# Optimization experiments

Hardware: AMD Instinct MI355X
Metric: run time of the kernel (lower is better)

Reference implementation:

```python
import jax, jax.numpy as jnp
import numpy as np

V, E, H, S = 32000, 1024, 1024, 2048


def setup_inputs() -> dict:
    key = jax.random.key(0)
    ks = jax.random.split(key, 16)
    std = 0.02
    return {
        "encoder_out": jax.random.normal(ks[0], (S, E), jnp.float32),
        "word_input": jax.random.randint(ks[1], (1,), 0, V, jnp.int32),
        "last_context": jax.random.normal(ks[2], (1, H), jnp.float32),
        "h0": jnp.zeros((1, 1, H), jnp.float32),
        "c0": jnp.zeros((1, 1, H), jnp.float32),
        # learned parameters
        "emb": jax.random.normal(ks[3], (V, E), jnp.float32) * std,
        "W_ih": jax.random.normal(ks[4], (4 * H, E + H), jnp.float32) * std,
        "W_hh": jax.random.normal(ks[5], (4 * H, H), jnp.float32) * std,
        "b_ih": jnp.zeros((4 * H,), jnp.float32),
        "b_hh": jnp.zeros((4 * H,), jnp.float32),
        "W_attn": jax.random.normal(ks[6], (H, E + H), jnp.float32) * std,
        "b_attn": jnp.zeros((H,), jnp.float32),
        "v": jax.random.uniform(ks[7], (H,), jnp.float32) * 0.1,
        "W_ah": jax.random.normal(ks[8], (H, E + H), jnp.float32) * std,
        "b_ah": jnp.zeros((H,), jnp.float32),
        "W_out": jax.random.normal(ks[9], (V, H), jnp.float32) * std,
        "b_out": jnp.zeros((V,), jnp.float32),
    }


def reference(encoder_out, word_input, last_context, h0, c0,
              emb, W_ih, W_hh, b_ih, b_hh,
              W_attn, b_attn, v, W_ah, b_ah, W_out, b_out):
    # single decoder step, batch=1 (dropout in eval mode == identity)
    embedded = emb[word_input[0]]                       # [E]
    x = jnp.concatenate([last_context[0], embedded])    # [H+E] (context first, as in torch.cat)
    # LSTM cell (PyTorch gate order i, f, g, o)
    gates = W_ih @ x + b_ih + W_hh @ h0[0, 0] + b_hh    # [4H]
    i, f, g, o = jnp.split(gates, 4)
    c = jax.nn.sigmoid(f) * c0[0, 0] + jax.nn.sigmoid(i) * jnp.tanh(g)
    ht = jax.nn.sigmoid(o) * jnp.tanh(c)                # [H]
    # additive attention, vectorized over encoder steps.
    # original concatenates (ht, encoder_out[i]); split attn weight accordingly.
    Wa_h, Wa_e = W_attn[:, :H], W_attn[:, H:]
    scores = jnp.tanh(encoder_out @ Wa_e.T + (Wa_h @ ht + b_attn)) @ v  # [S]
    w = jax.nn.softmax(scores)                          # [S]
    context = w @ encoder_out                           # [E]
    ht_tilda = jnp.tanh(W_ah @ jnp.concatenate([context, ht]) + b_ah)  # [H]
    output = jax.nn.log_softmax(W_out @ ht_tilda + b_out)              # [V]
    return (output[None, :], (ht[None, None, :], c[None, None, :]),
            ht_tilda[None, :], w[None, :])
```

## Files before the change

### kernel.cpp

```cpp
#include <hip/hip_runtime.h>
#include <math.h>

#define V_ 32000
#define E_ 1024
#define H_ 1024
#define S_ 2048

typedef __attribute__((ext_vector_type(8))) short bf16x8;
typedef __attribute__((ext_vector_type(8))) unsigned short u16x8;
typedef __attribute__((ext_vector_type(4))) float f32x4;

typedef __attribute__((address_space(1))) const unsigned int gu32;
typedef __attribute__((address_space(3))) unsigned int lu32;

__device__ __forceinline__ float sigmoidf_(float x) { return 1.0f / (1.0f + expf(-x)); }

__device__ __forceinline__ unsigned short f2bf(float f) {
    unsigned int u = __builtin_bit_cast(unsigned int, f);
    unsigned int r = (u + 0x7fffu + ((u >> 16) & 1u)) >> 16;
    return (unsigned short)r;
}
__device__ __forceinline__ float bf2f(unsigned short u) {
    return __builtin_bit_cast(float, ((unsigned int)u) << 16);
}
__device__ __forceinline__ u16x8 pack8(float4 a, float4 b) {
    u16x8 p;
    p[0] = f2bf(a.x); p[1] = f2bf(a.y); p[2] = f2bf(a.z); p[3] = f2bf(a.w);
    p[4] = f2bf(b.x); p[5] = f2bf(b.y); p[6] = f2bf(b.z); p[7] = f2bf(b.w);
    return p;
}
__device__ __forceinline__ void gload16(const void* g, void* l) {
    __builtin_amdgcn_global_load_lds((gu32*)g, (lu32*)l, 16, 0, 0);
}

__global__ __launch_bounds__(256) void kA(
    const float* __restrict__ W_ih, const float* __restrict__ W_hh,
    const float* __restrict__ b_ih, const float* __restrict__ b_hh,
    const float* __restrict__ last_context, const float* __restrict__ emb,
    const int* __restrict__ word, const float* __restrict__ h0,
    const float* __restrict__ c0, const float* __restrict__ enc,
    const float* __restrict__ W_attn,
    float* __restrict__ out_ht, float* __restrict__ out_c,
    float* __restrict__ ws_ht, unsigned short* __restrict__ encb,
    unsigned short* __restrict__ wab, float* __restrict__ ws_ctx)
{
    int b = blockIdx.x, tid = threadIdx.x;
    int wave = tid >> 6, lane = tid & 63;
    if (b < 1024) {
        __shared__ float sbuf[4];
        int j = b;
        const float* embrow = emb + (size_t)word[0] * E_;
        int row = j + wave * H_;
        const float* wi = W_ih + (size_t)row * (E_ + H_);
        const float* wh = W_hh + (size_t)row * H_;
        float acc = 0.f;
        #pragma unroll
        for (int it = 0; it < 8; ++it) {
            int idx = (lane + it * 64) * 4;
            float4 wv = *(const float4*)(wi + idx);
            float4 xv = (idx < H_) ? *(const float4*)(last_context + idx)
                                   : *(const float4*)(embrow + (idx - H_));
            acc = fmaf(wv.x, xv.x, acc); acc = fmaf(wv.y, xv.y, acc);
            acc = fmaf(wv.z, xv.z, acc); acc = fmaf(wv.w, xv.w, acc);
        }
        #pragma unroll
        for (int it = 0; it < 4; ++it) {
            int idx = (lane + it * 64) * 4;
            float4 wv = *(const float4*)(wh + idx);
            float4 hv = *(const float4*)(h0 + idx);
            acc = fmaf(wv.x, hv.x, acc); acc = fmaf(wv.y, hv.y, acc);
            acc = fmaf(wv.z, hv.z, acc); acc = fmaf(wv.w, hv.w, acc);
        }
        #pragma unroll
        for (int m = 32; m; m >>= 1) acc += __shfl_down(acc, m, 64);
        if (lane == 0) sbuf[wave] = acc;
        __syncthreads();
        if (tid < 4 && b == 0) {
        }
        if (tid == 0) {
            float gi = sbuf[0] + b_ih[j]          + b_hh[j];
            float gf = sbuf[1] + b_ih[j + H_]     + b_hh[j + H_];
            float gg = sbuf[2] + b_ih[j + 2*H_]   + b_hh[j + 2*H_];
            float go = sbuf[3] + b_ih[j + 3*H_]   + b_hh[j + 3*H_];
            float c  = sigmoidf_(gf) * c0[j] + sigmoidf_(gi) * tanhf(gg);
            float ht = sigmoidf_(go) * tanhf(c);
            out_c[j]  = c;
            out_ht[j] = ht;
            ws_ht[j]  = ht;
        }
        if (b == 0) {
            ws_ctx[tid] = 0.f;
            ws_ctx[tid + 256] = 0.f;
            ws_ctx[tid + 512] = 0.f;
            ws_ctx[tid + 768] = 0.f;
        }
    } else {
        int cid = (b - 1024) * 256 + tid;
        const int ENC_CH = (S_ * E_) / 8;
        #pragma unroll
        for (int i = 0; i < 3; ++i) {
            int idx = cid + i * 131072;
            const float* src;
            unsigned short* dst;
            if (idx < ENC_CH) {
                src = enc + (size_t)idx * 8;
                dst = encb + (size_t)idx * 8;
            } else {
                int w = idx - ENC_CH;
                int h = w >> 7, off = (w & 127) * 8;
                src = W_attn + (size_t)h * (E_ + H_) + H_ + off;
                dst = wab + (size_t)h * E_ + off;
            }
            float4 a = *(const float4*)src;
            float4 bq = *(const float4*)(src + 4);
            *(u16x8*)dst = pack8(a, bq);
        }
    }
}

__global__ __launch_bounds__(64) void kB(
    const float* __restrict__ W_attn, const float* __restrict__ b_attn,
    const float* __restrict__ ht, float* __restrict__ q)
{
    int h = blockIdx.x;
    int lane = threadIdx.x;
    const float* row = W_attn + (size_t)h * (E_ + H_);
    float acc = 0.f;
    #pragma unroll
    for (int it = 0; it < 4; ++it) {
        int idx = (lane + it * 64) * 4;
        float4 wv = *(const float4*)(row + idx);
        float4 hv = *(const float4*)(ht + idx);
        acc = fmaf(wv.x, hv.x, acc); acc = fmaf(wv.y, hv.y, acc);
        acc = fmaf(wv.z, hv.z, acc); acc = fmaf(wv.w, hv.w, acc);
    }
    #pragma unroll
    for (int m = 32; m; m >>= 1) acc += __shfl_down(acc, m, 64);
    if (lane == 0) q[h] = acc + b_attn[h];
}

__global__ __launch_bounds__(256) void kC(
    const unsigned short* __restrict__ encb, const unsigned short* __restrict__ wab,
    const float* __restrict__ q, const float* __restrict__ v,
    float* __restrict__ spart)
{
    __shared__ unsigned short As[2][128 * 64];
    __shared__ unsigned short Bs[2][64 * 64];
    int s0 = blockIdx.x * 128, h0 = blockIdx.y * 64;
    int tid = threadIdx.x;
    int wave = tid >> 6, lane = tid & 63;
    int wr = (wave >> 1) * 64, wc = (wave & 1) * 32;

    int srow = tid >> 3;
    int lch  = ((tid & 7) ^ (srow & 7)) * 8;
    const unsigned short* aSrc[4];
    #pragma unroll
    for (int jj = 0; jj < 4; ++jj)
        aSrc[jj] = encb + (size_t)(s0 + jj * 32 + srow) * E_ + lch;
    const unsigned short* bSrc[2];
    #pragma unroll
    for (int jj = 0; jj < 2; ++jj)
        bSrc[jj] = wab + (size_t)(h0 + jj * 32 + srow) * E_ + lch;

    int fc = lane & 15, g = lane >> 4;
    int aRow[4], bRow[2], pc[2];
    #pragma unroll
    for (int m = 0; m < 4; ++m) aRow[m] = (wr + m * 16 + fc) * 64;
    #pragma unroll
    for (int n = 0; n < 2; ++n) bRow[n] = (wc + n * 16 + fc) * 64;
    #pragma unroll
    for (int kk = 0; kk < 2; ++kk) pc[kk] = ((kk * 4 + g) ^ (fc & 7)) * 8;

    f32x4 acc[4][2];
    #pragma unroll
    for (int m = 0; m < 4; ++m)
        #pragma unroll
        for (int n = 0; n < 2; ++n)
            acc[m][n] = (f32x4){0.f, 0.f, 0.f, 0.f};

    #pragma unroll
    for (int jj = 0; jj < 4; ++jj) gload16(aSrc[jj], &As[0][jj * 2048 + tid * 8]);
    #pragma unroll
    for (int jj = 0; jj < 2; ++jj) gload16(bSrc[jj], &Bs[0][jj * 2048 + tid * 8]);
    __syncthreads();

    int cur = 0;
    for (int t = 0; t < 16; ++t) {
        if (t < 15) {
            int k0 = (t + 1) * 64;
            #pragma unroll
            for (int jj = 0; jj < 4; ++jj)
                gload16(aSrc[jj] + k0, &As[cur ^ 1][jj * 2048 + tid * 8]);
            #pragma unroll
            for (int jj = 0; jj < 2; ++jj)
                gload16(bSrc[jj] + k0, &Bs[cur ^ 1][jj * 2048 + tid * 8]);
        }
        #pragma unroll
        for (int kk = 0; kk < 2; ++kk) {
            bf16x8 af[4], bf2[2];
            #pragma unroll
            for (int m = 0; m < 4; ++m) af[m] = *(const bf16x8*)&As[cur][aRow[m] + pc[kk]];
            #pragma unroll
            for (int n = 0; n < 2; ++n) bf2[n] = *(const bf16x8*)&Bs[cur][bRow[n] + pc[kk]];
            #pragma unroll
            for (int m = 0; m < 4; ++m)
                #pragma unroll
                for (int n = 0; n < 2; ++n)
                    acc[m][n] = __builtin_amdgcn_mfma_f32_16x16x32_bf16(
                        af[m], bf2[n], acc[m][n], 0, 0, 0);
        }
        __syncthreads();
        cur ^= 1;
    }

    float qv[2], vv[2];
    #pragma unroll
    for (int n = 0; n < 2; ++n) {
        int col = h0 + wc + n * 16 + fc;
        qv[n] = q[col];
        vv[n] = v[col];
    }
    int part = blockIdx.y * 2 + (wave & 1);
    #pragma unroll
    for (int m = 0; m < 4; ++m) {
        #pragma unroll
        for (int j = 0; j < 4; ++j) {
            float p = 0.f;
            #pragma unroll
            for (int n = 0; n < 2; ++n)
                p += tanhf(acc[m][n][j] + qv[n]) * vv[n];
            #pragma unroll
            for (int mask = 8; mask; mask >>= 1) p += __shfl_xor(p, mask, 64);
            if (fc == 0)
                spart[(size_t)(s0 + wr + m * 16 + g * 4 + j) * 32 + part] = p;
        }
    }
}

__global__ __launch_bounds__(256) void kD(
    const float* __restrict__ spart, const unsigned short* __restrict__ encb,
    float* __restrict__ expw, float* __restrict__ gpart, float* __restrict__ ctx)
{
    __shared__ float esh[16];
    int b = blockIdx.x, tid = threadIdx.x;
    int s0 = b * 16;
    int sl = tid >> 4, pp = tid & 15;
    float vsum = spart[(size_t)(s0 + sl) * 32 + pp]
               + spart[(size_t)(s0 + sl) * 32 + pp + 16];
    #pragma unroll
    for (int mask = 8; mask; mask >>= 1) vsum += __shfl_xor(vsum, mask, 64);
    if (pp == 0) {
        float e = expf(vsum);
        expw[s0 + sl] = e;
        esh[sl] = e;
    }
    __syncthreads();
    if (tid == 0) {
        float bs = 0.f;
        #pragma unroll
        for (int i = 0; i < 16; ++i) bs += esh[i];
        gpart[b] = bs;
    }
    int e0 = tid * 4;
    float a0 = 0.f, a1 = 0.f, a2 = 0.f, a3 = 0.f;
    #pragma unroll
    for (int ss = 0; ss < 16; ++ss) {
        const unsigned short* r = encb + (size_t)(s0 + ss) * E_ + e0;
        ushort4 u = *(const ushort4*)r;
        float w = esh[ss];
        a0 = fmaf(w, bf2f(u.x), a0);
        a1 = fmaf(w, bf2f(u.y), a1);
        a2 = fmaf(w, bf2f(u.z), a2);
        a3 = fmaf(w, bf2f(u.w), a3);
    }
    atomicAdd(&ctx[e0 + 0], a0);
    atomicAdd(&ctx[e0 + 1], a1);
    atomicAdd(&ctx[e0 + 2], a2);
    atomicAdd(&ctx[e0 + 3], a3);
}

__global__ __launch_bounds__(64) void kE(
    const float* __restrict__ W_ah, const float* __restrict__ b_ah,
    const float* __restrict__ ctx, const float* __restrict__ ht,
    const float* __restrict__ gpart, const float* __restrict__ expw,
    float* __restrict__ out_htt, float* __restrict__ ws_htt,
    float* __restrict__ out_w)
{
    int b = blockIdx.x;
    int lane = threadIdx.x;
    float gsum = gpart[lane] + gpart[lane + 64];
    #pragma unroll
    for (int m = 32; m; m >>= 1) gsum += __shfl_xor(gsum, m, 64);
    float invS = 1.0f / gsum;
    if (b >= 1024) {
        int s = (b - 1024) * 256 + lane * 4;
        float4 e4 = *(const float4*)(expw + s);
        float4 w4 = { e4.x * invS, e4.y * invS, e4.z * invS, e4.w * invS };
        *(float4*)(out_w + s) = w4;
        return;
    }
    const float* row = W_ah + (size_t)b * (E_ + H_);
    float acc = 0.f;
    #pragma unroll
    for (int it = 0; it < 8; ++it) {
        int idx = (lane + it * 64) * 4;
        float4 wv = *(const float4*)(row + idx);
        float4 xv;
        if (idx < E_) {
            float4 cv = *(const float4*)(ctx + idx);
            xv = (float4){ cv.x * invS, cv.y * invS, cv.z * invS, cv.w * invS };
        } else {
            xv = *(const float4*)(ht + idx - E_);
        }
        acc = fmaf(wv.x, xv.x, acc); acc = fmaf(wv.y, xv.y, acc);
        acc = fmaf(wv.z, xv.z, acc); acc = fmaf(wv.w, xv.w, acc);
    }
    #pragma unroll
    for (int m = 32; m; m >>= 1) acc += __shfl_down(acc, m, 64);
    if (lane == 0) {
        float val = tanhf(acc + b_ah[b]);
        out_htt[b] = val;
        ws_htt[b]  = val;
    }
}

__global__ __launch_bounds__(256) void kF(
    const float* __restrict__ W_out, const float* __restrict__ b_out,
    const float* __restrict__ ht_tilda, float* __restrict__ logits,
    float* __restrict__ lpart)
{
    __shared__ float wes[4];
    int b = blockIdx.x;
    int wave = threadIdx.x >> 6, lane = threadIdx.x & 63;
    int row = b * 4 + wave;
    const float* wr = W_out + (size_t)row * H_;
    float acc = 0.f;
    #pragma unroll
    for (int it = 0; it < 4; ++it) {
        int idx = (lane + it * 64) * 4;
        float4 wv = *(const float4*)(wr + idx);
        float4 hv = *(const float4*)(ht_tilda + idx);
        acc = fmaf(wv.x, hv.x, acc); acc = fmaf(wv.y, hv.y, acc);
        acc = fmaf(wv.z, hv.z, acc); acc = fmaf(wv.w, hv.w, acc);
    }
    #pragma unroll
    for (int m = 32; m; m >>= 1) acc += __shfl_down(acc, m, 64);
    if (lane == 0) {
        float lg = acc + b_out[row];
        logits[row] = lg;
        wes[wave] = expf(lg);
    }
    __syncthreads();
    if (threadIdx.x == 0)
        lpart[b] = wes[0] + wes[1] + wes[2] + wes[3];
}

__global__ __launch_bounds__(256) void kG(
    float* __restrict__ out, const float* __restrict__ lpart)
{
    __shared__ float sred[4];
    int tid = threadIdx.x;
    float s = 0.f;
    for (int i = tid; i < 8000; i += 256) s += lpart[i];
    #pragma unroll
    for (int m = 32; m; m >>= 1) s += __shfl_down(s, m, 64);
    if ((tid & 63) == 0) sred[tid >> 6] = s;
    __syncthreads();
    float lse = logf(sred[0] + sred[1] + sred[2] + sred[3]);
    out[blockIdx.x * 256 + tid] -= lse;
}

extern "C" void kernel_launch(void* const* d_in, const int* in_sizes, int n_in,
                              void* d_out, int out_size, void* d_ws, size_t ws_size,
                              hipStream_t stream) {
    const float* enc          = (const float*)d_in[0];
    const int*   word         = (const int*)  d_in[1];
    const float* last_context = (const float*)d_in[2];
    const float* h0           = (const float*)d_in[3];
    const float* c0           = (const float*)d_in[4];
    const float* emb          = (const float*)d_in[5];
    const float* W_ih         = (const float*)d_in[6];
    const float* W_hh         = (const float*)d_in[7];
    const float* b_ih         = (const float*)d_in[8];
    const float* b_hh         = (const float*)d_in[9];
    const float* W_attn       = (const float*)d_in[10];
    const float* b_attn       = (const float*)d_in[11];
    const float* v            = (const float*)d_in[12];
    const float* W_ah         = (const float*)d_in[13];
    const float* b_ah         = (const float*)d_in[14];
    const float* W_out        = (const float*)d_in[15];
    const float* b_out        = (const float*)d_in[16];

    float* out        = (float*)d_out;
    float* out_logits = out;
    float* out_ht     = out + V_;
    float* out_c      = out + V_ + H_;
    float* out_htt    = out + V_ + 2 * H_;
    float* out_w      = out + V_ + 3 * H_;

    float* ws      = (float*)d_ws;
    float* ws_ht   = ws;
    float* ws_q    = ws + 1024;
    float* ws_expw = ws + 2048;
    float* ws_ctx  = ws + 4096;
    float* ws_htt  = ws + 5120;
    float* ws_gp   = ws + 6144;
    float* ws_lp   = ws + 8192;
    float* ws_sp   = ws + 16384;
    unsigned short* encb = (unsigned short*)(ws + 81920);
    unsigned short* wab  = encb + (size_t)S_ * E_;

    kA<<<1536, 256, 0, stream>>>(W_ih, W_hh, b_ih, b_hh, last_context, emb, word,
                                 h0, c0, enc, W_attn, out_ht, out_c, ws_ht,
                                 encb, wab, ws_ctx);
    kB<<<1024, 64, 0, stream>>>(W_attn, b_attn, ws_ht, ws_q);
    kC<<<dim3(S_ / 128, H_ / 64), 256, 0, stream>>>(encb, wab, ws_q, v, ws_sp);
    kD<<<128, 256, 0, stream>>>(ws_sp, encb, ws_expw, ws_gp, ws_ctx);
    kE<<<1032, 64, 0, stream>>>(W_ah, b_ah, ws_ctx, ws_ht, ws_gp, ws_expw,
                                out_htt, ws_htt, out_w);
    kF<<<8000, 256, 0, stream>>>(W_out, b_out, ws_htt, out_logits, ws_lp);
    kG<<<125, 256, 0, stream>>>(out_logits, ws_lp);
}
```

Before: 92.11 us.

## Fuse decoder stages into fewer kernels using atomic-counter grid barriers

```diff
diff --git a/kernel.cpp b/kernel.cpp
--- a/kernel.cpp
+++ b/kernel.cpp
@@ -31,6 +31,20 @@
 }
 __device__ __forceinline__ void gload16(const void* g, void* l) {
     __builtin_amdgcn_global_load_lds((gu32*)g, (lu32*)l, 16, 0, 0);
+}
+
+__device__ __forceinline__ void phase_release(unsigned int* ctr) {
+    __syncthreads();
+    if (threadIdx.x == 0)
+        __hip_atomic_fetch_add(ctr, 1u, __ATOMIC_RELEASE, __HIP_MEMORY_SCOPE_AGENT);
+}
+__device__ __forceinline__ void phase_acquire(unsigned int* ctr, unsigned int n) {
+    if (threadIdx.x == 0) {
+        while (__hip_atomic_load(ctr, __ATOMIC_ACQUIRE, __HIP_MEMORY_SCOPE_AGENT) < n)
+            __builtin_amdgcn_s_sleep(8);
+    }
+    __syncthreads();
+    __builtin_amdgcn_fence(__ATOMIC_ACQUIRE, "agent");
 }
 
 __global__ __launch_bounds__(256) void kA(
@@ -42,7 +56,8 @@
     const float* __restrict__ W_attn,
     float* __restrict__ out_ht, float* __restrict__ out_c,
     float* __restrict__ ws_ht, unsigned short* __restrict__ encb,
-    unsigned short* __restrict__ wab, float* __restrict__ ws_ctx)
+    unsigned short* __restrict__ wab, float* __restrict__ ws_ctx,
+    unsigned int* __restrict__ syncs)
 {
     int b = blockIdx.x, tid = threadIdx.x;
     int wave = tid >> 6, lane = tid & 63;
@@ -75,8 +90,6 @@
         for (int m = 32; m; m >>= 1) acc += __shfl_down(acc, m, 64);
         if (lane == 0) sbuf[wave] = acc;
         __syncthreads();
-        if (tid < 4 && b == 0) {
-        }
         if (tid == 0) {
             float gi = sbuf[0] + b_ih[j]          + b_hh[j];
             float gf = sbuf[1] + b_ih[j + H_]     + b_hh[j + H_];
@@ -89,10 +102,11 @@
             ws_ht[j]  = ht;
         }
         if (b == 0) {
-            ws_ctx[tid] = 0.f;
+            ws_ctx[tid]       = 0.f;
             ws_ctx[tid + 256] = 0.f;
             ws_ctx[tid + 512] = 0.f;
             ws_ctx[tid + 768] = 0.f;
+            if (tid < 8) syncs[tid] = 0u;
         }
     } else {
         int cid = (b - 1024) * 256 + tid;
@@ -118,39 +132,40 @@
     }
 }
 
-__global__ __launch_bounds__(64) void kB(
+__global__ __launch_bounds__(256) void kBC(
     const float* __restrict__ W_attn, const float* __restrict__ b_attn,
-    const float* __restrict__ ht, float* __restrict__ q)
-{
-    int h = blockIdx.x;
-    int lane = threadIdx.x;
-    const float* row = W_attn + (size_t)h * (E_ + H_);
-    float acc = 0.f;
-    #pragma unroll
-    for (int it = 0; it < 4; ++it) {
-        int idx = (lane + it * 64) * 4;
-        float4 wv = *(const float4*)(row + idx);
-        float4 hv = *(const float4*)(ht + idx);
-        acc = fmaf(wv.x, hv.x, acc); acc = fmaf(wv.y, hv.y, acc);
-        acc = fmaf(wv.z, hv.z, acc); acc = fmaf(wv.w, hv.w, acc);
-    }
-    #pragma unroll
-    for (int m = 32; m; m >>= 1) acc += __shfl_down(acc, m, 64);
-    if (lane == 0) q[h] = acc + b_attn[h];
-}
-
-__global__ __launch_bounds__(256) void kC(
+    const float* __restrict__ ws_ht,
     const unsigned short* __restrict__ encb, const unsigned short* __restrict__ wab,
-    const float* __restrict__ q, const float* __restrict__ v,
-    float* __restrict__ spart)
+    const float* __restrict__ v,
+    float* __restrict__ ws_q, float* __restrict__ spart,
+    unsigned int* __restrict__ syncs)
 {
     __shared__ unsigned short As[2][128 * 64];
     __shared__ unsigned short Bs[2][64 * 64];
-    int s0 = blockIdx.x * 128, h0 = blockIdx.y * 64;
+    int bx = blockIdx.x, by = blockIdx.y;
+    int b = by * 16 + bx;
     int tid = threadIdx.x;
     int wave = tid >> 6, lane = tid & 63;
-    int wr = (wave >> 1) * 64, wc = (wave & 1) * 32;
-
+
+    {
+        int r = b * 4 + wave;
+        const float* rowp = W_attn + (size_t)r * (E_ + H_);
+        float acc = 0.f;
+        #pragma unroll
+        for (int it = 0; it < 4; ++it) {
+            int idx = (lane + it * 64) * 4;
+            float4 wv = *(const float4*)(rowp + idx);
+            float4 hv = *(const float4*)(ws_ht + idx);
+            acc = fmaf(wv.x, hv.x, acc); acc = fmaf(wv.y, hv.y, acc);
+            acc = fmaf(wv.z, hv.z, acc); acc = fmaf(wv.w, hv.w, acc);
+        }
+        #pragma unroll
+        for (int m = 32; m; m >>= 1) acc += __shfl_down(acc, m, 64);
+        if (lane == 0) ws_q[r] = acc + b_attn[r];
+    }
+    phase_release(&syncs[0]);
+
+    int s0 = bx * 128, h0 = by * 64;
     int srow = tid >> 3;
     int lch  = ((tid & 7) ^ (srow & 7)) * 8;
     const unsigned short* aSrc[4];
@@ -162,6 +177,7 @@
     for (int jj = 0; jj < 2; ++jj)
         bSrc[jj] = wab + (size_t)(h0 + jj * 32 + srow) * E_ + lch;
 
+    int wr = (wave >> 1) * 64, wc = (wave & 1) * 32;
     int fc = lane & 15, g = lane >> 4;
     int aRow[4], bRow[2], pc[2];
     #pragma unroll
@@ -213,14 +229,16 @@
         cur ^= 1;
     }
 
+    phase_acquire(&syncs[0], 256u);
+
     float qv[2], vv[2];
     #pragma unroll
     for (int n = 0; n < 2; ++n) {
         int col = h0 + wc + n * 16 + fc;
-        qv[n] = q[col];
+        qv[n] = ws_q[col];
         vv[n] = v[col];
     }
-    int part = blockIdx.y * 2 + (wave & 1);
+    int part = by * 2 + (wave & 1);
     #pragma unroll
     for (int m = 0; m < 4; ++m) {
         #pragma unroll
@@ -237,36 +255,36 @@
     }
 }
 
-__global__ __launch_bounds__(256) void kD(
+__global__ __launch_bounds__(256) void kDE(
     const float* __restrict__ spart, const unsigned short* __restrict__ encb,
-    float* __restrict__ expw, float* __restrict__ gpart, float* __restrict__ ctx)
+    const float* __restrict__ W_ah, const float* __restrict__ b_ah,
+    const float* __restrict__ ws_ht,
+    float* __restrict__ gpart, float* __restrict__ ctx,
+    float* __restrict__ out_htt, float* __restrict__ ws_htt,
+    float* __restrict__ out_w, unsigned int* __restrict__ syncs)
 {
-    __shared__ float esh[16];
+    __shared__ float esh[8];
+    __shared__ float sred[4];
     int b = blockIdx.x, tid = threadIdx.x;
-    int s0 = b * 16;
-    int sl = tid >> 4, pp = tid & 15;
-    float vsum = spart[(size_t)(s0 + sl) * 32 + pp]
-               + spart[(size_t)(s0 + sl) * 32 + pp + 16];
-    #pragma unroll
-    for (int mask = 8; mask; mask >>= 1) vsum += __shfl_xor(vsum, mask, 64);
-    if (pp == 0) {
-        float e = expf(vsum);
-        expw[s0 + sl] = e;
-        esh[sl] = e;
-    }
+    int wave = tid >> 6, lane = tid & 63;
+    int s0 = b * 8;
+    int sl = tid >> 5, pp = tid & 31;
+    float vsum = spart[(size_t)(s0 + sl) * 32 + pp];
+    #pragma unroll
+    for (int m = 16; m; m >>= 1) vsum += __shfl_xor(vsum, m, 64);
+    if (pp == 0) esh[sl] = expf(vsum);
     __syncthreads();
     if (tid == 0) {
         float bs = 0.f;
         #pragma unroll
-        for (int i = 0; i < 16; ++i) bs += esh[i];
+        for (int i = 0; i < 8; ++i) bs += esh[i];
         gpart[b] = bs;
     }
     int e0 = tid * 4;
     float a0 = 0.f, a1 = 0.f, a2 = 0.f, a3 = 0.f;
     #pragma unroll
-    for (int ss = 0; ss < 16; ++ss) {
-        const unsigned short* r = encb + (size_t)(s0 + ss) * E_ + e0;
-        ushort4 u = *(const ushort4*)r;
+    for (int ss = 0; ss < 8; ++ss) {
+        ushort4 u = *(const ushort4*)(encb + (size_t)(s0 + ss) * E_ + e0);
         float w = esh[ss];
         a0 = fmaf(w, bf2f(u.x), a0);
         a1 = fmaf(w, bf2f(u.y), a1);
@@ -277,97 +295,87 @@
     atomicAdd(&ctx[e0 + 1], a1);
     atomicAdd(&ctx[e0 + 2], a2);
     atomicAdd(&ctx[e0 + 3], a3);
-}
-
-__global__ __launch_bounds__(64) void kE(
-    const float* __restrict__ W_ah, const float* __restrict__ b_ah,
-    const float* __restrict__ ctx, const float* __restrict__ ht,
-    const float* __restrict__ gpart, const float* __restrict__ expw,
-    float* __restrict__ out_htt, float* __restrict__ ws_htt,
-    float* __restrict__ out_w)
-{
-    int b = blockIdx.x;
-    int lane = threadIdx.x;
-    float gsum = gpart[lane] + gpart[lane + 64];
-    #pragma unroll
-    for (int m = 32; m; m >>= 1) gsum += __shfl_xor(gsum, m, 64);
-    float invS = 1.0f / gsum;
-    if (b >= 1024) {
-        int s = (b - 1024) * 256 + lane * 4;
-        float4 e4 = *(const float4*)(expw + s);
-        float4 w4 = { e4.x * invS, e4.y * invS, e4.z * invS, e4.w * invS };
-        *(float4*)(out_w + s) = w4;
-        return;
-    }
-    const float* row = W_ah + (size_t)b * (E_ + H_);
-    float acc = 0.f;
-    #pragma unroll
-    for (int it = 0; it < 8; ++it) {
-        int idx = (lane + it * 64) * 4;
-        float4 wv = *(const float4*)(row + idx);
-        float4 xv;
-        if (idx < E_) {
-            float4 cv = *(const float4*)(ctx + idx);
-            xv = (float4){ cv.x * invS, cv.y * invS, cv.z * invS, cv.w * invS };
-        } else {
-            xv = *(const float4*)(ht + idx - E_);
-        }
-        acc = fmaf(wv.x, xv.x, acc); acc = fmaf(wv.y, xv.y, acc);
-        acc = fmaf(wv.z, xv.z, acc); acc = fmaf(wv.w, xv.w, acc);
-    }
-    #pragma unroll
-    for (int m = 32; m; m >>= 1) acc += __shfl_down(acc, m, 64);
-    if (lane == 0) {
-        float val = tanhf(acc + b_ah[b]);
-        out_htt[b] = val;
-        ws_htt[b]  = val;
-    }
-}
-
-__global__ __launch_bounds__(256) void kF(
+    phase_release(&syncs[1]);
+    phase_acquire(&syncs[1], 256u);
+    float gv = gpart[tid];
+    #pragma unroll
+    for (int m = 32; m; m >>= 1) gv += __shfl_xor(gv, m, 64);
+    if (lane == 0) sred[wave] = gv;
+    __syncthreads();
+    float invS = 1.0f / (sred[0] + sred[1] + sred[2] + sred[3]);
+    {
+        int r = b * 4 + wave;
+        const float* rowp = W_ah + (size_t)r * (E_ + H_);
+        float acc = 0.f;
+        #pragma unroll
+        for (int it = 0; it < 8; ++it) {
+            int idx = (lane + it * 64) * 4;
+            float4 wv = *(const float4*)(rowp + idx);
+            float4 xv;
+            if (idx < E_) {
+                float4 cv = *(const float4*)(ctx + idx);
+                xv = (float4){ cv.x * invS, cv.y * invS, cv.z * invS, cv.w * invS };
+            } else {
+                xv = *(const float4*)(ws_ht + idx - E_);
+            }
+            acc = fmaf(wv.x, xv.x, acc); acc = fmaf(wv.y, xv.y, acc);
+            acc = fmaf(wv.z, xv.z, acc); acc = fmaf(wv.w, xv.w, acc);
+        }
+        #pragma unroll
+        for (int m = 32; m; m >>= 1) acc += __shfl_down(acc, m, 64);
+        if (lane == 0) {
+            float val = tanhf(acc + b_ah[r]);
+            out_htt[r] = val;
+            ws_htt[r]  = val;
+        }
+    }
+    if (tid < 8) out_w[s0 + tid] = esh[tid] * invS;
+}
+
+__global__ __launch_bounds__(256, 4) void kFG(
     const float* __restrict__ W_out, const float* __restrict__ b_out,
-    const float* __restrict__ ht_tilda, float* __restrict__ logits,
-    float* __restrict__ lpart)
+    const float* __restrict__ htt, float* __restrict__ logits,
+    unsigned int* __restrict__ syncs)
 {
     __shared__ float wes[4];
-    int b = blockIdx.x;
-    int wave = threadIdx.x >> 6, lane = threadIdx.x & 63;
-    int row = b * 4 + wave;
-    const float* wr = W_out + (size_t)row * H_;
-    float acc = 0.f;
-    #pragma unroll
-    for (int it = 0; it < 4; ++it) {
-        int idx = (lane + it * 64) * 4;
-        float4 wv = *(const float4*)(wr + idx);
-        float4 hv = *(const float4*)(ht_tilda + idx);
-        acc = fmaf(wv.x, hv.x, acc); acc = fmaf(wv.y, hv.y, acc);
-        acc = fmaf(wv.z, hv.z, acc); acc = fmaf(wv.w, hv.w, acc);
-    }
-    #pragma unroll
-    for (int m = 32; m; m >>= 1) acc += __shfl_down(acc, m, 64);
-    if (lane == 0) {
-        float lg = acc + b_out[row];
-        logits[row] = lg;
-        wes[wave] = expf(lg);
-    }
-    __syncthreads();
-    if (threadIdx.x == 0)
-        lpart[b] = wes[0] + wes[1] + wes[2] + wes[3];
-}
-
-__global__ __launch_bounds__(256) void kG(
-    float* __restrict__ out, const float* __restrict__ lpart)
-{
-    __shared__ float sred[4];
-    int tid = threadIdx.x;
-    float s = 0.f;
-    for (int i = tid; i < 8000; i += 256) s += lpart[i];
-    #pragma unroll
-    for (int m = 32; m; m >>= 1) s += __shfl_down(s, m, 64);
-    if ((tid & 63) == 0) sred[tid >> 6] = s;
-    __syncthreads();
-    float lse = logf(sred[0] + sred[1] + sred[2] + sred[3]);
-    out[blockIdx.x * 256 + tid] -= lse;
+    __shared__ float slse;
+    int b = blockIdx.x, tid = threadIdx.x;
+    int wave = tid >> 6, lane = tid & 63;
+    float esum = 0.f;
+    #pragma unroll
+    for (int k = 0; k < 8; ++k) {
+        int row = b * 32 + wave * 8 + k;
+        const float* wr = W_out + (size_t)row * H_;
+        float acc = 0.f;
+        #pragma unroll
+        for (int it = 0; it < 4; ++it) {
+            int idx = (lane + it * 64) * 4;
+            float4 wv = *(const float4*)(wr + idx);
+            float4 hv = *(const float4*)(htt + idx);
+            acc = fmaf(wv.x, hv.x, acc); acc = fmaf(wv.y, hv.y, acc);
+            acc = fmaf(wv.z, hv.z, acc); acc = fmaf(wv.w, hv.w, acc);
+        }
+        #pragma unroll
+        for (int m = 32; m; m >>= 1) acc += __shfl_down(acc, m, 64);
+        if (lane == 0) {
+            float lg = acc + b_out[row];
+            logits[row] = lg;
+            esum += expf(lg);
+        }
+    }
+    if (lane == 0) wes[wave] = esum;
+    __syncthreads();
+    if (tid == 0) {
+        float bs = wes[0] + wes[1] + wes[2] + wes[3];
+        atomicAdd((float*)&syncs[4], bs);
+        __hip_atomic_fetch_add(&syncs[2], 1u, __ATOMIC_RELEASE, __HIP_MEMORY_SCOPE_AGENT);
+        while (__hip_atomic_load(&syncs[2], __ATOMIC_ACQUIRE, __HIP_MEMORY_SCOPE_AGENT) < 1000u)
+            __builtin_amdgcn_s_sleep(8);
+        float gsl = __hip_atomic_load((float*)&syncs[4], __ATOMIC_RELAXED, __HIP_MEMORY_SCOPE_AGENT);
+        slse = logf(gsl);
+    }
+    __syncthreads();
+    if (tid < 32) logits[b * 32 + tid] -= slse;
 }
 
 extern "C" void kernel_launch(void* const* d_in, const int* in_sizes, int n_in,
@@ -398,26 +406,23 @@
     float* out_htt    = out + V_ + 2 * H_;
     float* out_w      = out + V_ + 3 * H_;
 
-    float* ws      = (float*)d_ws;
-    float* ws_ht   = ws;
-    float* ws_q    = ws + 1024;
-    float* ws_expw = ws + 2048;
-    float* ws_ctx  = ws + 4096;
-    float* ws_htt  = ws + 5120;
-    float* ws_gp   = ws + 6144;
-    float* ws_lp   = ws + 8192;
-    float* ws_sp   = ws + 16384;
+    float* ws       = (float*)d_ws;
+    float* ws_ht    = ws;
+    float* ws_q     = ws + 1024;
+    float* ws_htt   = ws + 2048;
+    float* ws_gp    = ws + 3072;
+    float* ws_ctx   = ws + 3328;
+    unsigned int* syncs = (unsigned int*)(ws + 4352);
+    float* ws_sp    = ws + 8192;
     unsigned short* encb = (unsigned short*)(ws + 81920);
     unsigned short* wab  = encb + (size_t)S_ * E_;
 
     kA<<<1536, 256, 0, stream>>>(W_ih, W_hh, b_ih, b_hh, last_context, emb, word,
                                  h0, c0, enc, W_attn, out_ht, out_c, ws_ht,
-                                 encb, wab, ws_ctx);
-    kB<<<1024, 64, 0, stream>>>(W_attn, b_attn, ws_ht, ws_q);
-    kC<<<dim3(S_ / 128, H_ / 64), 256, 0, stream>>>(encb, wab, ws_q, v, ws_sp);
-    kD<<<128, 256, 0, stream>>>(ws_sp, encb, ws_expw, ws_gp, ws_ctx);
-    kE<<<1032, 64, 0, stream>>>(W_ah, b_ah, ws_ctx, ws_ht, ws_gp, ws_expw,
-                                out_htt, ws_htt, out_w);
-    kF<<<8000, 256, 0, stream>>>(W_out, b_out, ws_htt, out_logits, ws_lp);
-    kG<<<125, 256, 0, stream>>>(out_logits, ws_lp);
-}
+                                 encb, wab, ws_ctx, syncs);
+    kBC<<<dim3(16, 16), 256, 0, stream>>>(W_attn, b_attn, ws_ht, encb, wab, v,
+                                          ws_q, ws_sp, syncs);
+    kDE<<<256, 256, 0, stream>>>(ws_sp, encb, W_ah, b_ah, ws_ht,
+                                 ws_gp, ws_ctx, out_htt, ws_htt, out_w, syncs);
+    kFG<<<1000, 256, 0, stream>>>(W_out, b_out, ws_htt, out_logits, syncs);
+}
```

New measurement: 278.5 us. 202% more time.

## Fuse attention query projection into score GEMM and widen output-projection rows per wave

Applied to the files above, without the earlier changes.

```diff
diff --git a/kernel.cpp b/kernel.cpp
--- a/kernel.cpp
+++ b/kernel.cpp
@@ -75,8 +75,6 @@
         for (int m = 32; m; m >>= 1) acc += __shfl_down(acc, m, 64);
         if (lane == 0) sbuf[wave] = acc;
         __syncthreads();
-        if (tid < 4 && b == 0) {
-        }
         if (tid == 0) {
             float gi = sbuf[0] + b_ih[j]          + b_hh[j];
             float gf = sbuf[1] + b_ih[j + H_]     + b_hh[j + H_];
@@ -89,7 +87,7 @@
             ws_ht[j]  = ht;
         }
         if (b == 0) {
-            ws_ctx[tid] = 0.f;
+            ws_ctx[tid]       = 0.f;
             ws_ctx[tid + 256] = 0.f;
             ws_ctx[tid + 512] = 0.f;
             ws_ctx[tid + 768] = 0.f;
@@ -118,111 +116,97 @@
     }
 }
 
-__global__ __launch_bounds__(64) void kB(
+__global__ __launch_bounds__(256) void kC(
     const float* __restrict__ W_attn, const float* __restrict__ b_attn,
-    const float* __restrict__ ht, float* __restrict__ q)
-{
-    int h = blockIdx.x;
-    int lane = threadIdx.x;
-    const float* row = W_attn + (size_t)h * (E_ + H_);
-    float acc = 0.f;
-    #pragma unroll
-    for (int it = 0; it < 4; ++it) {
-        int idx = (lane + it * 64) * 4;
-        float4 wv = *(const float4*)(row + idx);
-        float4 hv = *(const float4*)(ht + idx);
-        acc = fmaf(wv.x, hv.x, acc); acc = fmaf(wv.y, hv.y, acc);
-        acc = fmaf(wv.z, hv.z, acc); acc = fmaf(wv.w, hv.w, acc);
-    }
-    #pragma unroll
-    for (int m = 32; m; m >>= 1) acc += __shfl_down(acc, m, 64);
-    if (lane == 0) q[h] = acc + b_attn[h];
-}
-
-__global__ __launch_bounds__(256) void kC(
+    const float* __restrict__ ws_ht,
     const unsigned short* __restrict__ encb, const unsigned short* __restrict__ wab,
-    const float* __restrict__ q, const float* __restrict__ v,
-    float* __restrict__ spart)
-{
-    __shared__ unsigned short As[2][128 * 64];
-    __shared__ unsigned short Bs[2][64 * 64];
-    int s0 = blockIdx.x * 128, h0 = blockIdx.y * 64;
+    const float* __restrict__ v, float* __restrict__ spart)
+{
+    __shared__ unsigned short As[64 * 64];
+    __shared__ unsigned short Bs[64 * 64];
+    __shared__ float qsh[64], vsh[64];
+    int bx = blockIdx.x, by = blockIdx.y;
+    int s0 = bx * 64, h0 = by * 64;
     int tid = threadIdx.x;
     int wave = tid >> 6, lane = tid & 63;
-    int wr = (wave >> 1) * 64, wc = (wave & 1) * 32;
-
-    int srow = tid >> 3;
-    int lch  = ((tid & 7) ^ (srow & 7)) * 8;
-    const unsigned short* aSrc[4];
-    #pragma unroll
-    for (int jj = 0; jj < 4; ++jj)
-        aSrc[jj] = encb + (size_t)(s0 + jj * 32 + srow) * E_ + lch;
-    const unsigned short* bSrc[2];
-    #pragma unroll
-    for (int jj = 0; jj < 2; ++jj)
-        bSrc[jj] = wab + (size_t)(h0 + jj * 32 + srow) * E_ + lch;
-
+
+    #pragma unroll 1
+    for (int i = 0; i < 16; ++i) {
+        int r = h0 + wave * 16 + i;
+        const float* rowp = W_attn + (size_t)r * (E_ + H_);
+        float acc = 0.f;
+        #pragma unroll
+        for (int it = 0; it < 4; ++it) {
+            int idx = (lane + it * 64) * 4;
+            float4 wv = *(const float4*)(rowp + idx);
+            float4 hv = *(const float4*)(ws_ht + idx);
+            acc = fmaf(wv.x, hv.x, acc); acc = fmaf(wv.y, hv.y, acc);
+            acc = fmaf(wv.z, hv.z, acc); acc = fmaf(wv.w, hv.w, acc);
+        }
+        #pragma unroll
+        for (int m = 32; m; m >>= 1) acc += __shfl_down(acc, m, 64);
+        if (lane == 0) qsh[wave * 16 + i] = acc + b_attn[r];
+    }
+    if (tid < 64) vsh[tid] = v[h0 + tid];
+
+    int r0 = tid >> 3, p0 = tid & 7;
+    int lc = (p0 ^ (r0 & 7)) * 8;
+    const unsigned short* aS0 = encb + (size_t)(s0 + r0) * E_ + lc;
+    const unsigned short* aS1 = encb + (size_t)(s0 + 32 + r0) * E_ + lc;
+    const unsigned short* bS0 = wab  + (size_t)(h0 + r0) * E_ + lc;
+    const unsigned short* bS1 = wab  + (size_t)(h0 + 32 + r0) * E_ + lc;
+
+    int wr = (wave >> 1) * 32, wc = (wave & 1) * 32;
     int fc = lane & 15, g = lane >> 4;
-    int aRow[4], bRow[2], pc[2];
-    #pragma unroll
-    for (int m = 0; m < 4; ++m) aRow[m] = (wr + m * 16 + fc) * 64;
+    int aRow[2], bRow[2], pc[2];
+    #pragma unroll
+    for (int m = 0; m < 2; ++m) aRow[m] = (wr + m * 16 + fc) * 64;
     #pragma unroll
     for (int n = 0; n < 2; ++n) bRow[n] = (wc + n * 16 + fc) * 64;
     #pragma unroll
     for (int kk = 0; kk < 2; ++kk) pc[kk] = ((kk * 4 + g) ^ (fc & 7)) * 8;
 
-    f32x4 acc[4][2];
-    #pragma unroll
-    for (int m = 0; m < 4; ++m)
+    f32x4 acc[2][2];
+    #pragma unroll
+    for (int m = 0; m < 2; ++m)
         #pragma unroll
         for (int n = 0; n < 2; ++n)
             acc[m][n] = (f32x4){0.f, 0.f, 0.f, 0.f};
 
-    #pragma unroll
-    for (int jj = 0; jj < 4; ++jj) gload16(aSrc[jj], &As[0][jj * 2048 + tid * 8]);
-    #pragma unroll
-    for (int jj = 0; jj < 2; ++jj) gload16(bSrc[jj], &Bs[0][jj * 2048 + tid * 8]);
-    __syncthreads();
-
-    int cur = 0;
     for (int t = 0; t < 16; ++t) {
-        if (t < 15) {
-            int k0 = (t + 1) * 64;
+        int k0 = t * 64;
+        gload16(aS0 + k0, As + tid * 8);
+        gload16(aS1 + k0, As + (tid + 256) * 8);
+        gload16(bS0 + k0, Bs + tid * 8);
+        gload16(bS1 + k0, Bs + (tid + 256) * 8);
+        __syncthreads();
+        #pragma unroll
+        for (int kk = 0; kk < 2; ++kk) {
+            bf16x8 af[2], bf2[2];
             #pragma unroll
-            for (int jj = 0; jj < 4; ++jj)
-                gload16(aSrc[jj] + k0, &As[cur ^ 1][jj * 2048 + tid * 8]);
+            for (int m = 0; m < 2; ++m) af[m] = *(const bf16x8*)(As + aRow[m] + pc[kk]);
             #pragma unroll
-            for (int jj = 0; jj < 2; ++jj)
-                gload16(bSrc[jj] + k0, &Bs[cur ^ 1][jj * 2048 + tid * 8]);
-        }
-        #pragma unroll
-        for (int kk = 0; kk < 2; ++kk) {
-            bf16x8 af[4], bf2[2];
+            for (int n = 0; n < 2; ++n) bf2[n] = *(const bf16x8*)(Bs + bRow[n] + pc[kk]);
             #pragma unroll
-            for (int m = 0; m < 4; ++m) af[m] = *(const bf16x8*)&As[cur][aRow[m] + pc[kk]];
-            #pragma unroll
-            for (int n = 0; n < 2; ++n) bf2[n] = *(const bf16x8*)&Bs[cur][bRow[n] + pc[kk]];
-            #pragma unroll
-            for (int m = 0; m < 4; ++m)
+            for (int m = 0; m < 2; ++m)
                 #pragma unroll
                 for (int n = 0; n < 2; ++n)
                     acc[m][n] = __builtin_amdgcn_mfma_f32_16x16x32_bf16(
                         af[m], bf2[n], acc[m][n], 0, 0, 0);
         }
         __syncthreads();
-        cur ^= 1;
     }
 
     float qv[2], vv[2];
     #pragma unroll
     for (int n = 0; n < 2; ++n) {
-        int col = h0 + wc + n * 16 + fc;
-        qv[n] = q[col];
-        vv[n] = v[col];
-    }
-    int part = blockIdx.y * 2 + (wave & 1);
-    #pragma unroll
-    for (int m = 0; m < 4; ++m) {
+        int col = wc + n * 16 + fc;
+        qv[n] = qsh[col];
+        vv[n] = vsh[col];
+    }
+    int part = by * 2 + (wave & 1);
+    #pragma unroll
+    for (int m = 0; m < 2; ++m) {
         #pragma unroll
         for (int j = 0; j < 4; ++j) {
             float p = 0.f;
@@ -265,8 +249,7 @@
     float a0 = 0.f, a1 = 0.f, a2 = 0.f, a3 = 0.f;
     #pragma unroll
     for (int ss = 0; ss < 16; ++ss) {
-        const unsigned short* r = encb + (size_t)(s0 + ss) * E_ + e0;
-        ushort4 u = *(const ushort4*)r;
+        ushort4 u = *(const ushort4*)(encb + (size_t)(s0 + ss) * E_ + e0);
         float w = esh[ss];
         a0 = fmaf(w, bf2f(u.x), a0);
         a1 = fmaf(w, bf2f(u.y), a1);
@@ -332,42 +315,62 @@
     __shared__ float wes[4];
     int b = blockIdx.x;
     int wave = threadIdx.x >> 6, lane = threadIdx.x & 63;
-    int row = b * 4 + wave;
-    const float* wr = W_out + (size_t)row * H_;
-    float acc = 0.f;
+    int r0 = b * 8 + wave * 2;
+    const float* w0 = W_out + (size_t)r0 * H_;
+    const float* w1 = W_out + (size_t)(r0 + 1) * H_;
+    float a0 = 0.f, a1 = 0.f;
     #pragma unroll
     for (int it = 0; it < 4; ++it) {
         int idx = (lane + it * 64) * 4;
-        float4 wv = *(const float4*)(wr + idx);
         float4 hv = *(const float4*)(ht_tilda + idx);
-        acc = fmaf(wv.x, hv.x, acc); acc = fmaf(wv.y, hv.y, acc);
-        acc = fmaf(wv.z, hv.z, acc); acc = fmaf(wv.w, hv.w, acc);
-    }
-    #pragma unroll
-    for (int m = 32; m; m >>= 1) acc += __shfl_down(acc, m, 64);
+        float4 v0 = *(const float4*)(w0 + idx);
+        float4 v1 = *(const float4*)(w1 + idx);
+        a0 = fmaf(v0.x, hv.x, a0); a0 = fmaf(v0.y, hv.y, a0);
+        a0 = fmaf(v0.z, hv.z, a0); a0 = fmaf(v0.w, hv.w, a0);
+        a1 = fmaf(v1.x, hv.x, a1); a1 = fmaf(v1.y, hv.y, a1);
+        a1 = fmaf(v1.z, hv.z, a1); a1 = fmaf(v1.w, hv.w, a1);
+    }
+    #pragma unroll
+    for (int m = 32; m; m >>= 1) {
+        a0 += __shfl_down(a0, m, 64);
+        a1 += __shfl_down(a1, m, 64);
+    }
     if (lane == 0) {
-        float lg = acc + b_out[row];
-        logits[row] = lg;
-        wes[wave] = expf(lg);
+        float lg0 = a0 + b_out[r0];
+        float lg1 = a1 + b_out[r0 + 1];
+        logits[r0]     = lg0;
+        logits[r0 + 1] = lg1;
+        wes[wave] = expf(lg0) + expf(lg1);
     }
     __syncthreads();
     if (threadIdx.x == 0)
         lpart[b] = wes[0] + wes[1] + wes[2] + wes[3];
 }
 
-__global__ __launch_bounds__(256) void kG(
+__global__ __launch_bounds__(1024) void kG(
     float* __restrict__ out, const float* __restrict__ lpart)
 {
-    __shared__ float sred[4];
-    int tid = threadIdx.x;
+    __shared__ float sred[16];
+    int b = blockIdx.x, tid = threadIdx.x;
     float s = 0.f;
-    for (int i = tid; i < 8000; i += 256) s += lpart[i];
+    #pragma unroll
+    for (int k = 0; k < 4; ++k) {
+        int i = tid + k * 1024;
+        if (i < 4000) s += lpart[i];
+    }
     #pragma unroll
     for (int m = 32; m; m >>= 1) s += __shfl_down(s, m, 64);
     if ((tid & 63) == 0) sred[tid >> 6] = s;
     __syncthreads();
-    float lse = logf(sred[0] + sred[1] + sred[2] + sred[3]);
-    out[blockIdx.x * 256 + tid] -= lse;
+    float tot = 0.f;
+    #pragma unroll
+    for (int i = 0; i < 16; ++i) tot += sred[i];
+    float lse = logf(tot);
+    #pragma unroll
+    for (int k = 0; k < 4; ++k) {
+        int row = b * 4000 + k * 1024 + tid;
+        if (row < (b + 1) * 4000 && row < V_) out[row] -= lse;
+    }
 }
 
 extern "C" void kernel_launch(void* const* d_in, const int* in_sizes, int n_in,
@@ -400,12 +403,11 @@
 
     float* ws      = (float*)d_ws;
     float* ws_ht   = ws;
-    float* ws_q    = ws + 1024;
-    float* ws_expw = ws + 2048;
-    float* ws_ctx  = ws + 4096;
-    float* ws_htt  = ws + 5120;
-    float* ws_gp   = ws + 6144;
-    float* ws_lp   = ws + 8192;
+    float* ws_expw = ws + 1024;
+    float* ws_ctx  = ws + 3072;
+    float* ws_gp   = ws + 4096;
+    float* ws_htt  = ws + 4224;
+    float* ws_lp   = ws + 5248;
     float* ws_sp   = ws + 16384;
     unsigned short* encb = (unsigned short*)(ws + 81920);
     unsigned short* wab  = encb + (size_t)S_ * E_;
@@ -413,11 +415,10 @@
     kA<<<1536, 256, 0, stream>>>(W_ih, W_hh, b_ih, b_hh, last_context, emb, word,
                                  h0, c0, enc, W_attn, out_ht, out_c, ws_ht,
                                  encb, wab, ws_ctx);
-    kB<<<1024, 64, 0, stream>>>(W_attn, b_attn, ws_ht, ws_q);
-    kC<<<dim3(S_ / 128, H_ / 64), 256, 0, stream>>>(encb, wab, ws_q, v, ws_sp);
+    kC<<<dim3(32, 16), 256, 0, stream>>>(W_attn, b_attn, ws_ht, encb, wab, v, ws_sp);
     kD<<<128, 256, 0, stream>>>(ws_sp, encb, ws_expw, ws_gp, ws_ctx);
     kE<<<1032, 64, 0, stream>>>(W_ah, b_ah, ws_ctx, ws_ht, ws_gp, ws_expw,
                                 out_htt, ws_htt, out_w);
-    kF<<<8000, 256, 0, stream>>>(W_out, b_out, ws_htt, out_logits, ws_lp);
-    kG<<<125, 256, 0, stream>>>(out_logits, ws_lp);
-}
+    kF<<<4000, 256, 0, stream>>>(W_out, b_out, ws_htt, out_logits, ws_lp);
+    kG<<<8, 1024, 0, stream>>>(out_logits, ws_lp);
+}
```

Measured after the change: 84.87 us. -7.9%, faster.
